# Optimization experiments

Hardware: AMD Instinct MI355X
Metric: run time of the kernel (lower is better)

## Reference

```python
import jax, jax.numpy as jnp
import numpy as np

H = 1024   # hidden_size
A = 512    # attention_dim
C = 1000   # num_classes
NB = 5     # branches: l, r, f2l, f2r, h2h
IN = 42    # 21 landmarks * 2 coords per branch


def setup_inputs() -> dict:
    key = jax.random.key(0)
    ks = jax.random.split(key, 17)
    s = 0.02
    def n(k, shape):
        return jax.random.normal(k, shape, dtype=jnp.float32) * s
    return {
        "x": jax.random.normal(ks[0], (1, 133, 2), dtype=jnp.float32),
        # layer-0 LSTM params, stacked over the 5 branches (PyTorch gate order i,f,g,o)
        "W_ih0": n(ks[1], (NB, 4 * H, IN)),
        "W_hh0": n(ks[2], (NB, 4 * H, H)),
        "b_ih0": n(ks[3], (NB, 4 * H)),
        "b_hh0": n(ks[4], (NB, 4 * H)),
        # layer-1 LSTM params
        "W_ih1": n(ks[5], (NB, 4 * H, H)),
        "W_hh1": n(ks[6], (NB, 4 * H, H)),
        "b_ih1": n(ks[7], (NB, 4 * H)),
        "b_hh1": n(ks[8], (NB, 4 * H)),
        # per-branch additive attention
        "Wa": n(ks[9], (NB, A, H)),
        "ba": n(ks[10], (NB, A)),
        "Ws": n(ks[11], (NB, A)),
        "bs": n(ks[12], (NB,)),
        # fusion + classifier
        "fuse_w": n(ks[13], (H, NB * H)),
        "fuse_b": n(ks[14], (H,)),
        "fc_w": n(ks[15], (C, H)),
        "fc_b": n(ks[16], (C,)),
    }


def _prepare_input(x):
    # x: (1, 133, 2) -> (5, 42) branch features. Mirrors prepare_input exactly.
    x0 = x[0]
    body = x0[:17]
    left = x0[91:112]
    right = x0[112:133]
    src_body = x0[0]
    src_left = x0[100]
    src_right = x0[121]
    w_l = left[:, 0].max() - left[:, 0].min()
    h_l = left[:, 1].max() - left[:, 1].min()
    w_r = right[:, 0].max() - right[:, 0].min()
    h_r = right[:, 1].max() - right[:, 1].min()
    w_b = body[5, 0] - body[6, 0]
    h_b = 4.0 * w_b
    f2l = left - src_body
    f2r = right - src_body
    h2h = left - right
    left = left - src_left
    right = right - src_right
    one = jnp.ones((), x.dtype)
    cond_l = (w_l != 0) & (h_l != 0)
    cond_r = (w_r != 0) & (h_r != 0)
    cond_b = (w_b != 0) & (h_b != 0)
    left = left / jnp.stack([jnp.where(cond_l, w_l, one), jnp.where(cond_l, h_l, one)])
    right = right / jnp.stack([jnp.where(cond_r, w_r, one), jnp.where(cond_r, h_r, one)])
    wb = jnp.where(cond_b, w_b, one)
    hb = jnp.where(cond_b, h_b, one)
    f2l = f2l / jnp.stack([wb, one])   # only x-column divided by w_body
    f2r = f2r / jnp.stack([one, hb])   # only y-column divided by h_body
    h2h = h2h / jnp.stack([wb, hb])
    feat = jnp.concatenate([left, right, f2l, f2r, h2h], axis=0)  # (105, 2)
    return feat.reshape(NB, IN)  # split the 210-vector into the 5 branch slices


def _lstm_cell(xi, h, c, Wih, Whh, bih, bhh):
    g = Wih @ xi + bih + Whh @ h + bhh            # (4H,)
    i, f, gg, o = jnp.split(g, 4)
    c2 = jax.nn.sigmoid(f) * c + jax.nn.sigmoid(i) * jnp.tanh(gg)
    h2 = jax.nn.sigmoid(o) * jnp.tanh(c2)
    return h2


def _branch(xi, Wih0, Whh0, bih0, bhh0, Wih1, Whh1, bih1, bhh1, Wa_, ba_, Ws_, bs_):
    z = jnp.zeros((H,), xi.dtype)  # initialize_cell_and_hidden_state -> zeros
    h0 = _lstm_cell(xi, z, z, Wih0, Whh0, bih0, bhh0)
    h1 = _lstm_cell(h0, z, z, Wih1, Whh1, bih1, bhh1)
    # additive attention over the length-1 sequence (softmax over 1 elem == 1)
    aw = jnp.tanh(Wa_ @ h1 + ba_)                 # (A,)
    s = Ws_ @ aw + bs_                            # scalar score
    w = jax.nn.softmax(s.reshape(1))[0]
    return w * h1                                 # context vector (H,)


def _forward(x, W_ih0, W_hh0, b_ih0, b_hh0, W_ih1, W_hh1, b_ih1, b_hh1,
             Wa, ba, Ws, bs, fuse_w, fuse_b, fc_w, fc_b):
    xb = _prepare_input(x)                        # (5, 42)
    ctx = jax.vmap(_branch)(xb, W_ih0, W_hh0, b_ih0, b_hh0,
                            W_ih1, W_hh1, b_ih1, b_hh1, Wa, ba, Ws, bs)  # (5, H)
    fused = fuse_w @ ctx.reshape(NB * H) + fuse_b # (H,)
    logits = fc_w @ fused + fc_b                  # (C,)
    return logits[None, :]                        # (1, C)


def reference(x, W_ih0, W_hh0, b_ih0, b_hh0, W_ih1, W_hh1, b_ih1, b_hh1,
              Wa, ba, Ws, bs, fuse_w, fuse_b, fc_w, fc_b):
    return _forward(x, W_ih0, W_hh0, b_ih0, b_hh0, W_ih1, W_hh1, b_ih1, b_hh1,
                    Wa, ba, Ws, bs, fuse_w, fuse_b, fc_w, fc_b)
```

## Files before the change

kernel.cpp:

```cpp
#include <hip/hip_runtime.h>
#include <math.h>

#define H 1024
#define NB 5
#define IN 42
#define C_OUT 1000

__device__ __forceinline__ float sigmoidf_(float x) {
    return 1.0f / (1.0f + expf(-x));
}

__device__ __forceinline__ float wave_reduce_sum(float v) {
    #pragma unroll
    for (int off = 32; off > 0; off >>= 1) v += __shfl_xor(v, off);
    return v;
}

__global__ void layer0_kernel(const float* __restrict__ x,
                              const float* __restrict__ wih0,
                              const float* __restrict__ bih0,
                              const float* __restrict__ bhh0,
                              float* __restrict__ h0out) {
    __shared__ float slx[21], sly[21], srx[21], sry[21];
    __shared__ float sxb[IN];

    int out0 = blockIdx.x * 4;
    int b = out0 >> 10;

    int t = threadIdx.x;
    if (t < 21) {
        slx[t] = x[(91 + t) * 2 + 0];
        sly[t] = x[(91 + t) * 2 + 1];
        srx[t] = x[(112 + t) * 2 + 0];
        sry[t] = x[(112 + t) * 2 + 1];
    }
    __syncthreads();

    if (t < 21) {
        float lx_min = slx[0], lx_max = slx[0], ly_min = sly[0], ly_max = sly[0];
        float rx_min = srx[0], rx_max = srx[0], ry_min = sry[0], ry_max = sry[0];
        #pragma unroll
        for (int i = 1; i < 21; ++i) {
            lx_min = fminf(lx_min, slx[i]); lx_max = fmaxf(lx_max, slx[i]);
            ly_min = fminf(ly_min, sly[i]); ly_max = fmaxf(ly_max, sly[i]);
            rx_min = fminf(rx_min, srx[i]); rx_max = fmaxf(rx_max, srx[i]);
            ry_min = fminf(ry_min, sry[i]); ry_max = fmaxf(ry_max, sry[i]);
        }
        float w_l = lx_max - lx_min, h_l = ly_max - ly_min;
        float w_r = rx_max - rx_min, h_r = ry_max - ry_min;
        float w_b = x[5 * 2 + 0] - x[6 * 2 + 0];
        float h_b = 4.0f * w_b;
        float sbx = x[0], sby = x[1];
        float slx0 = slx[9], sly0 = sly[9];
        float srx0 = srx[9], sry0 = sry[9];
        bool cond_l = (w_l != 0.0f) && (h_l != 0.0f);
        bool cond_r = (w_r != 0.0f) && (h_r != 0.0f);
        bool cond_b = (w_b != 0.0f) && (h_b != 0.0f);
        float dlx = cond_l ? w_l : 1.0f, dly = cond_l ? h_l : 1.0f;
        float drx = cond_r ? w_r : 1.0f, dry = cond_r ? h_r : 1.0f;
        float wb  = cond_b ? w_b : 1.0f, hb  = cond_b ? h_b : 1.0f;

        float lx = slx[t], ly = sly[t], rx = srx[t], ry = sry[t];
        float vx, vy;
        switch (b) {
            case 0: vx = (lx - slx0) / dlx; vy = (ly - sly0) / dly; break;
            case 1: vx = (rx - srx0) / drx; vy = (ry - sry0) / dry; break;
            case 2: vx = (lx - sbx) / wb;   vy = (ly - sby);        break;
            case 3: vx = (rx - sbx);        vy = (ry - sby) / hb;   break;
            default:vx = (lx - rx) / wb;    vy = (ly - ry) / hb;    break;
        }
        sxb[2 * t + 0] = vx;
        sxb[2 * t + 1] = vy;
    }
    __syncthreads();

    int wave = t >> 6;
    int lane = t & 63;
    int j = (out0 + wave) & (H - 1);

    float xv = (lane < IN) ? sxb[lane] : 0.0f;
    const float* Wb = wih0 + (size_t)b * 4 * H * IN;
    float gi = 0.0f, gg = 0.0f, go = 0.0f;
    if (lane < IN) {
        gi = Wb[(size_t)(j)         * IN + lane] * xv;
        gg = Wb[(size_t)(j + 2 * H) * IN + lane] * xv;
        go = Wb[(size_t)(j + 3 * H) * IN + lane] * xv;
    }
    gi = wave_reduce_sum(gi);
    gg = wave_reduce_sum(gg);
    go = wave_reduce_sum(go);
    if (lane == 0) {
        size_t base = (size_t)b * 4 * H;
        gi += bih0[base + j]         + bhh0[base + j];
        gg += bih0[base + j + 2 * H] + bhh0[base + j + 2 * H];
        go += bih0[base + j + 3 * H] + bhh0[base + j + 3 * H];
        float c2 = sigmoidf_(gi) * tanhf(gg);
        h0out[b * H + j] = sigmoidf_(go) * tanhf(c2);
    }
}

__global__ void layer1_kernel(const float* __restrict__ wih1,
                              const float* __restrict__ bih1,
                              const float* __restrict__ bhh1,
                              const float* __restrict__ h0,
                              float* __restrict__ ctx) {
    __shared__ float4 hs[H / 4];
    int out0 = blockIdx.x * 8;
    int b = out0 >> 10;
    if (threadIdx.x < H / 4)
        hs[threadIdx.x] = ((const float4*)(h0 + b * H))[threadIdx.x];
    __syncthreads();

    int wave = threadIdx.x >> 6;
    int lane = threadIdx.x & 63;
    int j = (out0 + wave) & (H - 1);

    const float* Wb = wih1 + (size_t)b * 4 * H * H;
    const float4* ri = (const float4*)(Wb + (size_t)(j)         * H);
    const float4* rg = (const float4*)(Wb + (size_t)(j + 2 * H) * H);
    const float4* ro = (const float4*)(Wb + (size_t)(j + 3 * H) * H);

    float gi = 0.0f, gg = 0.0f, go = 0.0f;
    #pragma unroll
    for (int k = lane; k < H / 4; k += 64) {
        float4 h = hs[k];
        float4 a = ri[k]; gi += a.x * h.x + a.y * h.y + a.z * h.z + a.w * h.w;
        float4 c = rg[k]; gg += c.x * h.x + c.y * h.y + c.z * h.z + c.w * h.w;
        float4 d = ro[k]; go += d.x * h.x + d.y * h.y + d.z * h.z + d.w * h.w;
    }
    gi = wave_reduce_sum(gi);
    gg = wave_reduce_sum(gg);
    go = wave_reduce_sum(go);
    if (lane == 0) {
        size_t base = (size_t)b * 4 * H;
        gi += bih1[base + j]         + bhh1[base + j];
        gg += bih1[base + j + 2 * H] + bhh1[base + j + 2 * H];
        go += bih1[base + j + 3 * H] + bhh1[base + j + 3 * H];
        float c2 = sigmoidf_(gi) * tanhf(gg);
        ctx[b * H + j] = sigmoidf_(go) * tanhf(c2);
    }
}

__global__ void fuse_kernel(const float* __restrict__ fuse_w,
                            const float* __restrict__ fuse_b,
                            const float* __restrict__ ctx,
                            float* __restrict__ fused) {
    int row = blockIdx.x;
    const float4* r  = (const float4*)(fuse_w + (size_t)row * (NB * H));
    const float4* c4 = (const float4*)ctx;
    float acc = 0.0f;
    #pragma unroll
    for (int k = threadIdx.x; k < (NB * H) / 4; k += 256) {
        float4 a = r[k], c = c4[k];
        acc += a.x * c.x + a.y * c.y + a.z * c.z + a.w * c.w;
    }
    acc = wave_reduce_sum(acc);
    __shared__ float red[4];
    int wave = threadIdx.x >> 6, lane = threadIdx.x & 63;
    if (lane == 0) red[wave] = acc;
    __syncthreads();
    if (threadIdx.x == 0) {
        fused[row] = red[0] + red[1] + red[2] + red[3] + fuse_b[row];
    }
}

__global__ void fc_kernel(const float* __restrict__ fc_w,
                          const float* __restrict__ fc_b,
                          const float* __restrict__ fused,
                          float* __restrict__ out) {
    __shared__ float4 fs[H / 4];
    fs[threadIdx.x] = ((const float4*)fused)[threadIdx.x];
    __syncthreads();
    int wave = threadIdx.x >> 6, lane = threadIdx.x & 63;
    int row = blockIdx.x * 4 + wave;
    const float4* r = (const float4*)(fc_w + (size_t)row * H);
    float acc = 0.0f;
    #pragma unroll
    for (int k = lane; k < H / 4; k += 64) {
        float4 a = r[k], f = fs[k];
        acc += a.x * f.x + a.y * f.y + a.z * f.z + a.w * f.w;
    }
    acc = wave_reduce_sum(acc);
    if (lane == 0) out[row] = acc + fc_b[row];
}

extern "C" void kernel_launch(void* const* d_in, const int* in_sizes, int n_in,
                              void* d_out, int out_size, void* d_ws, size_t ws_size,
                              hipStream_t stream) {
    (void)in_sizes; (void)n_in; (void)out_size; (void)ws_size;
    const float* x      = (const float*)d_in[0];
    const float* W_ih0  = (const float*)d_in[1];
    const float* b_ih0  = (const float*)d_in[3];
    const float* b_hh0  = (const float*)d_in[4];
    const float* W_ih1  = (const float*)d_in[5];
    const float* b_ih1  = (const float*)d_in[7];
    const float* b_hh1  = (const float*)d_in[8];
    const float* fuse_w = (const float*)d_in[13];
    const float* fuse_b = (const float*)d_in[14];
    const float* fc_w   = (const float*)d_in[15];
    const float* fc_b   = (const float*)d_in[16];
    float* out = (float*)d_out;

    float* ws    = (float*)d_ws;
    float* h0    = ws;
    float* ctx   = ws + 5120;
    float* fused = ws + 10240;

    layer0_kernel<<<1280, 256, 0, stream>>>(x, W_ih0, b_ih0, b_hh0, h0);
    layer1_kernel<<<640, 512, 0, stream>>>(W_ih1, b_ih1, b_hh1, h0, ctx);
    fuse_kernel<<<1024, 256, 0, stream>>>(fuse_w, fuse_b, ctx, fused);
    fc_kernel<<<250, 256, 0, stream>>>(fc_w, fc_b, fused, out);
}
```

Measured before the change: 247.7 us.

## Fuse all four stages into one cooperative persistent kernel with grid syncs

New measurement: 536.5 us. +116.6%, slower.

```diff
diff --git a/kernel.cpp b/kernel.cpp
--- a/kernel.cpp
+++ b/kernel.cpp
@@ -1,5 +1,8 @@
 #include <hip/hip_runtime.h>
+#include <hip/hip_cooperative_groups.h>
 #include <math.h>
+
+namespace cg = cooperative_groups;
 
 #define H 1024
 #define NB 5
@@ -14,6 +17,172 @@
     #pragma unroll
     for (int off = 32; off > 0; off >>= 1) v += __shfl_xor(v, off);
     return v;
+}
+
+__global__ __launch_bounds__(256, 4)
+void mega_kernel(const float* __restrict__ x,
+                 const float* __restrict__ wih0,
+                 const float* __restrict__ bih0,
+                 const float* __restrict__ bhh0,
+                 const float* __restrict__ wih1,
+                 const float* __restrict__ bih1,
+                 const float* __restrict__ bhh1,
+                 const float* __restrict__ fuse_w,
+                 const float* __restrict__ fuse_b,
+                 const float* __restrict__ fc_w,
+                 const float* __restrict__ fc_b,
+                 float* __restrict__ h0,
+                 float* __restrict__ ctx,
+                 float* __restrict__ fused,
+                 float* __restrict__ out) {
+    cg::grid_group grid = cg::this_grid();
+
+    __shared__ float slx[21], sly[21], srx[21], sry[21];
+    __shared__ float sxb[NB * IN];
+    __shared__ float sred[4];
+
+    int t = threadIdx.x;
+    int wave = t >> 6;
+    int lane = t & 63;
+    int gw = blockIdx.x * 4 + wave;
+
+    if (t < 21) {
+        slx[t] = x[(91 + t) * 2 + 0];
+        sly[t] = x[(91 + t) * 2 + 1];
+        srx[t] = x[(112 + t) * 2 + 0];
+        sry[t] = x[(112 + t) * 2 + 1];
+    }
+    __syncthreads();
+    if (t < 21) {
+        float lx_min = slx[0], lx_max = slx[0], ly_min = sly[0], ly_max = sly[0];
+        float rx_min = srx[0], rx_max = srx[0], ry_min = sry[0], ry_max = sry[0];
+        #pragma unroll
+        for (int i = 1; i < 21; ++i) {
+            lx_min = fminf(lx_min, slx[i]); lx_max = fmaxf(lx_max, slx[i]);
+            ly_min = fminf(ly_min, sly[i]); ly_max = fmaxf(ly_max, sly[i]);
+            rx_min = fminf(rx_min, srx[i]); rx_max = fmaxf(rx_max, srx[i]);
+            ry_min = fminf(ry_min, sry[i]); ry_max = fmaxf(ry_max, sry[i]);
+        }
+        float w_l = lx_max - lx_min, h_l = ly_max - ly_min;
+        float w_r = rx_max - rx_min, h_r = ry_max - ry_min;
+        float w_b = x[5 * 2 + 0] - x[6 * 2 + 0];
+        float h_b = 4.0f * w_b;
+        float sbx = x[0], sby = x[1];
+        bool cond_l = (w_l != 0.0f) && (h_l != 0.0f);
+        bool cond_r = (w_r != 0.0f) && (h_r != 0.0f);
+        bool cond_b = (w_b != 0.0f) && (h_b != 0.0f);
+        float dlx = cond_l ? w_l : 1.0f, dly = cond_l ? h_l : 1.0f;
+        float drx = cond_r ? w_r : 1.0f, dry = cond_r ? h_r : 1.0f;
+        float wb  = cond_b ? w_b : 1.0f, hb  = cond_b ? h_b : 1.0f;
+
+        float lx = slx[t], ly = sly[t], rx = srx[t], ry = sry[t];
+        float slx0 = slx[9], sly0 = sly[9], srx0 = srx[9], sry0 = sry[9];
+        sxb[0 * IN + 2 * t + 0] = (lx - slx0) / dlx;
+        sxb[0 * IN + 2 * t + 1] = (ly - sly0) / dly;
+        sxb[1 * IN + 2 * t + 0] = (rx - srx0) / drx;
+        sxb[1 * IN + 2 * t + 1] = (ry - sry0) / dry;
+        sxb[2 * IN + 2 * t + 0] = (lx - sbx) / wb;
+        sxb[2 * IN + 2 * t + 1] = (ly - sby);
+        sxb[3 * IN + 2 * t + 0] = (rx - sbx);
+        sxb[3 * IN + 2 * t + 1] = (ry - sby) / hb;
+        sxb[4 * IN + 2 * t + 0] = (lx - rx) / wb;
+        sxb[4 * IN + 2 * t + 1] = (ly - ry) / hb;
+    }
+    __syncthreads();
+
+    #pragma unroll
+    for (int rep = 0; rep < 2; ++rep) {
+        int idx = gw + rep * 4096;
+        if (idx < NB * H) {
+            int b = idx >> 10;
+            int j = idx & (H - 1);
+            const float* Wb = wih0 + (size_t)b * 4 * H * IN;
+            float gi = 0.0f, gg = 0.0f, go = 0.0f;
+            if (lane < IN) {
+                float xv = sxb[b * IN + lane];
+                gi = Wb[(size_t)(j)         * IN + lane] * xv;
+                gg = Wb[(size_t)(j + 2 * H) * IN + lane] * xv;
+                go = Wb[(size_t)(j + 3 * H) * IN + lane] * xv;
+            }
+            gi = wave_reduce_sum(gi);
+            gg = wave_reduce_sum(gg);
+            go = wave_reduce_sum(go);
+            if (lane == 0) {
+                size_t base = (size_t)b * 4 * H;
+                gi += bih0[base + j]         + bhh0[base + j];
+                gg += bih0[base + j + 2 * H] + bhh0[base + j + 2 * H];
+                go += bih0[base + j + 3 * H] + bhh0[base + j + 3 * H];
+                float c2 = sigmoidf_(gi) * tanhf(gg);
+                h0[idx] = sigmoidf_(go) * tanhf(c2);
+            }
+        }
+    }
+    grid.sync();
+
+    #pragma unroll
+    for (int rep = 0; rep < 2; ++rep) {
+        int idx = gw + rep * 4096;
+        if (idx < NB * H) {
+            int b = idx >> 10;
+            int j = idx & (H - 1);
+            const float4* hb4 = (const float4*)(h0 + (size_t)b * H);
+            const float* Wb = wih1 + (size_t)b * 4 * H * H;
+            const float4* ri = (const float4*)(Wb + (size_t)(j)         * H);
+            const float4* rg = (const float4*)(Wb + (size_t)(j + 2 * H) * H);
+            const float4* ro = (const float4*)(Wb + (size_t)(j + 3 * H) * H);
+            float gi = 0.0f, gg = 0.0f, go = 0.0f;
+            #pragma unroll
+            for (int r = 0; r < 4; ++r) {
+                int k = lane + 64 * r;
+                float4 h4 = hb4[k];
+                float4 a = ri[k]; gi += a.x * h4.x + a.y * h4.y + a.z * h4.z + a.w * h4.w;
+                float4 c = rg[k]; gg += c.x * h4.x + c.y * h4.y + c.z * h4.z + c.w * h4.w;
+                float4 d = ro[k]; go += d.x * h4.x + d.y * h4.y + d.z * h4.z + d.w * h4.w;
+            }
+            gi = wave_reduce_sum(gi);
+            gg = wave_reduce_sum(gg);
+            go = wave_reduce_sum(go);
+            if (lane == 0) {
+                size_t base = (size_t)b * 4 * H;
+                gi += bih1[base + j]         + bhh1[base + j];
+                gg += bih1[base + j + 2 * H] + bhh1[base + j + 2 * H];
+                go += bih1[base + j + 3 * H] + bhh1[base + j + 3 * H];
+                float c2 = sigmoidf_(gi) * tanhf(gg);
+                ctx[idx] = sigmoidf_(go) * tanhf(c2);
+            }
+        }
+    }
+    grid.sync();
+
+    {
+        int row = blockIdx.x;
+        const float4* r4 = (const float4*)(fuse_w + (size_t)row * (NB * H));
+        const float4* c4 = (const float4*)ctx;
+        float acc = 0.0f;
+        #pragma unroll
+        for (int k = t; k < (NB * H) / 4; k += 256) {
+            float4 a = r4[k], c = c4[k];
+            acc += a.x * c.x + a.y * c.y + a.z * c.z + a.w * c.w;
+        }
+        acc = wave_reduce_sum(acc);
+        if (lane == 0) sred[wave] = acc;
+        __syncthreads();
+        if (t == 0) fused[row] = sred[0] + sred[1] + sred[2] + sred[3] + fuse_b[row];
+    }
+    grid.sync();
+
+    if (blockIdx.x < C_OUT) {
+        int row = blockIdx.x;
+        const float4* r4 = (const float4*)(fc_w + (size_t)row * H);
+        const float4* f4 = (const float4*)fused;
+        float4 a = r4[t];
+        float4 f = f4[t];
+        float acc = a.x * f.x + a.y * f.y + a.z * f.z + a.w * f.w;
+        acc = wave_reduce_sum(acc);
+        if (lane == 0) sred[wave] = acc;
+        __syncthreads();
+        if (t == 0) out[row] = sred[0] + sred[1] + sred[2] + sred[3] + fc_b[row];
+    }
 }
 
 __global__ void layer0_kernel(const float* __restrict__ x,
@@ -206,8 +375,19 @@
     float* ctx   = ws + 5120;
     float* fused = ws + 10240;
 
-    layer0_kernel<<<1280, 256, 0, stream>>>(x, W_ih0, b_ih0, b_hh0, h0);
-    layer1_kernel<<<640, 512, 0, stream>>>(W_ih1, b_ih1, b_hh1, h0, ctx);
-    fuse_kernel<<<1024, 256, 0, stream>>>(fuse_w, fuse_b, ctx, fused);
-    fc_kernel<<<250, 256, 0, stream>>>(fc_w, fc_b, fused, out);
-}
+    void* args[] = {
+        (void*)&x, (void*)&W_ih0, (void*)&b_ih0, (void*)&b_hh0,
+        (void*)&W_ih1, (void*)&b_ih1, (void*)&b_hh1,
+        (void*)&fuse_w, (void*)&fuse_b, (void*)&fc_w, (void*)&fc_b,
+        (void*)&h0, (void*)&ctx, (void*)&fused, (void*)&out
+    };
+    hipError_t rc = hipLaunchCooperativeKernel((const void*)mega_kernel,
+                                               dim3(1024), dim3(256),
+                                               args, 0, stream);
+    if (rc != hipSuccess) {
+        layer0_kernel<<<1280, 256, 0, stream>>>(x, W_ih0, b_ih0, b_hh0, h0);
+        layer1_kernel<<<640, 512, 0, stream>>>(W_ih1, b_ih1, b_hh1, h0, ctx);
+        fuse_kernel<<<1024, 256, 0, stream>>>(fuse_w, fuse_b, ctx, fused);
+        fc_kernel<<<250, 256, 0, stream>>>(fc_w, fc_b, fused, out);
+    }
+}
```
